# Performance work log

Measured on AMD Instinct MI355X. Metric: run time of the kernel, lower is better.

## Reference

```python
import jax, jax.numpy as jnp
import numpy as np

LN_EPS = 1e-5
SA_EPS = 1e-8
NUM_ITERS = 3

def layer_norm(x, w, b):
    mu = jnp.mean(x, axis=-1, keepdims=True)
    var = jnp.mean((x - mu) ** 2, axis=-1, keepdims=True)
    return (x - mu) / jnp.sqrt(var + LN_EPS) * w + b


def setup_inputs() -> dict:
    key = jax.random.key(0)
    ks = jax.random.split(key, 24)
    B, C, H, W = 128, 256, 32, 32
    D, S, MH, NC = 64, 8, 128, 15
    s = lambda k, shape, scale=0.02: jax.random.normal(k, shape, dtype=jnp.float32) * scale
    inp = {
        "x1": jax.random.normal(ks[0], (B, C, H, W), dtype=jnp.float32),
        "x2": jax.random.normal(ks[1], (B, C, H, W), dtype=jnp.float32),
        # 1x1 convs stored as [out,in]
        "conv1_w": s(ks[2], (D, C)), "conv1_b": jnp.zeros((D,), jnp.float32),
        "conv2_w": s(ks[3], (D, C)), "conv2_b": jnp.zeros((D,), jnp.float32),
        "norm_w": jnp.ones((D,), jnp.float32), "norm_b": jnp.zeros((D,), jnp.float32),
        "ni_w": jnp.ones((D,), jnp.float32), "ni_b": jnp.zeros((D,), jnp.float32),
        "ns_w": jnp.ones((D,), jnp.float32), "ns_b": jnp.zeros((D,), jnp.float32),
        "nm_w": jnp.ones((D,), jnp.float32), "nm_b": jnp.zeros((D,), jnp.float32),
        "slots_mu": s(ks[4], (1, 1, D), 1.0), "slots_log_sigma": s(ks[5], (1, 1, D), 0.1),
        "Wq": s(ks[6], (D, D), 0.1), "Wk": s(ks[7], (D, D), 0.1), "Wv": s(ks[8], (D, D), 0.1),
        "gru_wih": s(ks[9], (3 * D, D), 0.1), "gru_whh": s(ks[10], (3 * D, D), 0.1),
        "gru_bih": jnp.zeros((3 * D,), jnp.float32), "gru_bhh": jnp.zeros((3 * D,), jnp.float32),
        "mlp_w1": s(ks[11], (MH, D), 0.1), "mlp_b1": jnp.zeros((MH,), jnp.float32),
        "mlp_w2": s(ks[12], (D, MH), 0.1), "mlp_b2": jnp.zeros((D,), jnp.float32),
        "head_w": s(ks[13], (NC, D), 0.1), "head_b": jnp.zeros((NC,), jnp.float32),
        "noise": jax.random.normal(ks[14], (B, S, D), dtype=jnp.float32),
    }
    return inp


def _forward(x1, x2, conv1_w, conv1_b, conv2_w, conv2_b, norm_w, norm_b,
             ni_w, ni_b, ns_w, ns_b, nm_w, nm_b, slots_mu, slots_log_sigma,
             Wq, Wk, Wv, gru_wih, gru_whh, gru_bih, gru_bhh,
             mlp_w1, mlp_b1, mlp_w2, mlp_b2, head_w, head_b, noise):
    B = x1.shape[0]
    D = Wq.shape[0]
    # 1x1 convs then flatten to tokens: [B, H*W, D]
    t1 = jnp.einsum('bchw,dc->bhwd', x1, conv1_w).reshape(B, -1, D) + conv1_b
    t2 = jnp.einsum('bchw,dc->bhwd', x2, conv2_w).reshape(B, -1, D) + conv2_b
    inputs = jnp.concatenate([t1, t2], axis=1)          # [B, N, D]
    inputs = layer_norm(inputs, norm_w, norm_b)

    # SlotAttention
    inputs = layer_norm(inputs, ni_w, ni_b)
    k = inputs @ Wk.T                                    # [B, N, D]
    v = inputs @ Wv.T
    slots = slots_mu + jnp.exp(slots_log_sigma) * noise  # [B, S, D]
    scale = D ** -0.5
    for _ in range(NUM_ITERS):
        slots_prev = slots
        sn = layer_norm(slots, ns_w, ns_b)
        q = (sn @ Wq.T) * scale                          # [B, S, D]
        attn_logits = jnp.einsum('bnd,bsd->bns', k, q)   # [B, N, S]
        attn = jax.nn.softmax(attn_logits, axis=-1) + SA_EPS
        attn = attn / jnp.sum(attn, axis=-2, keepdims=True)
        updates = jnp.einsum('bns,bnd->bsd', attn, v)    # [B, S, D]
        # GRUCell (torch gate order: r, z, n)
        gi = updates @ gru_wih.T + gru_bih               # [B, S, 3D]
        gh = slots_prev @ gru_whh.T + gru_bhh
        ir, iz, inn = jnp.split(gi, 3, axis=-1)
        hr, hz, hn = jnp.split(gh, 3, axis=-1)
        r = jax.nn.sigmoid(ir + hr)
        z = jax.nn.sigmoid(iz + hz)
        n = jnp.tanh(inn + r * hn)
        slots = (1.0 - z) * n + z * slots_prev
        # residual MLP
        h = layer_norm(slots, nm_w, nm_b)
        h = jax.nn.relu(h @ mlp_w1.T + mlp_b1) @ mlp_w2.T + mlp_b2
        slots = slots + h

    fused = jnp.mean(slots, axis=1)                      # [B, D]
    return fused @ head_w.T + head_b                     # [B, n_classes]


def reference(x1, x2, conv1_w, conv1_b, conv2_w, conv2_b, norm_w, norm_b,
              ni_w, ni_b, ns_w, ns_b, nm_w, nm_b, slots_mu, slots_log_sigma,
              Wq, Wk, Wv, gru_wih, gru_whh, gru_bih, gru_bhh,
              mlp_w1, mlp_b1, mlp_w2, mlp_b2, head_w, head_b, noise):
    return _forward(x1, x2, conv1_w, conv1_b, conv2_w, conv2_b, norm_w, norm_b,
                    ni_w, ni_b, ns_w, ns_b, nm_w, nm_b, slots_mu, slots_log_sigma,
                    Wq, Wk, Wv, gru_wih, gru_whh, gru_bih, gru_bhh,
                    mlp_w1, mlp_b1, mlp_w2, mlp_b2, head_w, head_b, noise)
```

## Files before the change

kernel.cpp:

```cpp
#include <hip/hip_runtime.h>
#include <stdint.h>


typedef __bf16 bf16;
typedef __bf16 bf16x8 __attribute__((ext_vector_type(8)));
typedef float  f32x4  __attribute__((ext_vector_type(4)));

#define MFMA16(a, b, c) __builtin_amdgcn_mfma_f32_16x16x32_bf16((a), (b), (c), 0, 0, 0)

__global__ __launch_bounds__(256) void k0_convert(
    const float* __restrict__ c1w, const float* __restrict__ c2w,
    const float* __restrict__ wk,  const float* __restrict__ wvv,
    bf16* __restrict__ wconv, bf16* __restrict__ wkv)
{
  const int i = blockIdx.x * 256 + threadIdx.x;
  if (i < 16384) {
    wconv[i]         = (bf16)c1w[i];
    wconv[16384 + i] = (bf16)c2w[i];
  }
  if (i < 4096) {
    wkv[i]        = (bf16)wk[i];
    wkv[4096 + i] = (bf16)wvv[i];
  }
}

__global__ __launch_bounds__(256) void k1_conv_kv(
    const float* __restrict__ x1, const float* __restrict__ x2,
    const float* __restrict__ c1b, const float* __restrict__ c2b,
    const float* __restrict__ nw,  const float* __restrict__ nb,
    const float* __restrict__ niw, const float* __restrict__ nib,
    const bf16* __restrict__ wconv, const bf16* __restrict__ wkv,
    bf16* __restrict__ kbuf, bf16* __restrict__ vT)
{
  __shared__ union {
    struct { float T[64][65]; bf16 tok[64][72]; } p2;
    struct { float Tk[64][65]; float Tv[64][65]; } kv;
  } U;

  const int bx   = blockIdx.x;
  const int tile = bx & 15;
  const int img  = (bx >> 4) & 1;
  const int b    = bx >> 5;
  const int tid  = threadIdx.x;
  const int lane = tid & 63;
  const int wvid = tid >> 6;
  const int l15  = lane & 15;
  const int quad = lane >> 4;

  const float* xp = (img ? x2 : x1) + (size_t)b * (256 * 1024) + tile * 64;
  const bf16* wc  = wconv + img * (64 * 256);
  const int p     = wvid * 16 + l15;
  const float* xcol = xp + p + (size_t)quad * 8 * 1024;

  float xv[64];
  #pragma unroll
  for (int g = 0; g < 8; ++g)
    #pragma unroll
    for (int j = 0; j < 8; ++j)
      xv[g * 8 + j] = xcol[(size_t)(g * 32 + j) * 1024];

  f32x4 acc[4] = {{0.f,0.f,0.f,0.f},{0.f,0.f,0.f,0.f},{0.f,0.f,0.f,0.f},{0.f,0.f,0.f,0.f}};

  #pragma unroll
  for (int g = 0; g < 8; ++g) {
    bf16x8 af;
    #pragma unroll
    for (int j = 0; j < 8; ++j)
      af[j] = (bf16)xv[g * 8 + j];
    #pragma unroll
    for (int nt = 0; nt < 4; ++nt) {
      const bf16x8 bw = *(const bf16x8*)&wc[(nt * 16 + l15) * 256 + g * 32 + quad * 8];
      acc[nt] = MFMA16(af, bw, acc[nt]);
    }
  }

  {
    const float* cb = img ? c2b : c1b;
    #pragma unroll
    for (int nt = 0; nt < 4; ++nt) {
      const int d = nt * 16 + l15;
      const float bias = cb[d];
      #pragma unroll
      for (int r = 0; r < 4; ++r)
        U.p2.T[wvid * 16 + quad * 4 + r][d] = acc[nt][r] + bias;
    }
  }
  __syncthreads();

  {
    const int pix = tid >> 2, part = tid & 3;
    float xv2[16], yv[16];
    float s = 0.f, s2 = 0.f;
    #pragma unroll
    for (int i = 0; i < 16; ++i) {
      xv2[i] = U.p2.T[pix][part * 16 + i];
      s += xv2[i]; s2 += xv2[i] * xv2[i];
    }
    s  += __shfl_xor(s, 1);  s  += __shfl_xor(s, 2);
    s2 += __shfl_xor(s2, 1); s2 += __shfl_xor(s2, 2);
    float mu   = s * 0.015625f;
    float rstd = rsqrtf(s2 * 0.015625f - mu * mu + 1e-5f);
    s = 0.f; s2 = 0.f;
    #pragma unroll
    for (int i = 0; i < 16; ++i) {
      const int d = part * 16 + i;
      const float y = (xv2[i] - mu) * rstd * nw[d] + nb[d];
      yv[i] = y; s += y; s2 += y * y;
    }
    s  += __shfl_xor(s, 1);  s  += __shfl_xor(s, 2);
    s2 += __shfl_xor(s2, 1); s2 += __shfl_xor(s2, 2);
    mu   = s * 0.015625f;
    rstd = rsqrtf(s2 * 0.015625f - mu * mu + 1e-5f);
    #pragma unroll
    for (int i = 0; i < 16; ++i) {
      const int d = part * 16 + i;
      U.p2.tok[pix][d] = (bf16)((yv[i] - mu) * rstd * niw[d] + nib[d]);
    }
  }
  __syncthreads();

  f32x4 ak[4] = {{0.f,0.f,0.f,0.f},{0.f,0.f,0.f,0.f},{0.f,0.f,0.f,0.f},{0.f,0.f,0.f,0.f}};
  f32x4 av[4] = {{0.f,0.f,0.f,0.f},{0.f,0.f,0.f,0.f},{0.f,0.f,0.f,0.f},{0.f,0.f,0.f,0.f}};
  #pragma unroll
  for (int k0 = 0; k0 < 64; k0 += 32) {
    const bf16x8 af = *(const bf16x8*)&U.p2.tok[wvid * 16 + l15][k0 + quad * 8];
    #pragma unroll
    for (int nt = 0; nt < 4; ++nt) {
      const bf16x8 bk = *(const bf16x8*)&wkv[(nt * 16 + l15) * 64 + k0 + quad * 8];
      const bf16x8 bv = *(const bf16x8*)&wkv[4096 + (nt * 16 + l15) * 64 + k0 + quad * 8];
      ak[nt] = MFMA16(af, bk, ak[nt]);
      av[nt] = MFMA16(af, bv, av[nt]);
    }
  }
  __syncthreads();

  #pragma unroll
  for (int nt = 0; nt < 4; ++nt)
    #pragma unroll
    for (int r = 0; r < 4; ++r) {
      U.kv.Tk[wvid * 16 + quad * 4 + r][nt * 16 + l15] = ak[nt][r];
      U.kv.Tv[nt * 16 + l15][wvid * 16 + quad * 4 + r] = av[nt][r];
    }
  __syncthreads();
  {
    const int row = tid >> 2, dd = (tid & 3) * 16;
    const size_t kb = ((size_t)b * 2048 + img * 1024 + tile * 64) * 64;
    bf16 tb[16];
    #pragma unroll
    for (int i = 0; i < 16; ++i) tb[i] = (bf16)U.kv.Tk[row][dd + i];
    *(bf16x8*)&kbuf[kb + (size_t)row * 64 + dd]     = *(bf16x8*)&tb[0];
    *(bf16x8*)&kbuf[kb + (size_t)row * 64 + dd + 8] = *(bf16x8*)&tb[8];
    #pragma unroll
    for (int i = 0; i < 16; ++i) tb[i] = (bf16)U.kv.Tv[row][dd + i];
    const size_t vb = ((size_t)b * 64 + row) * 2048 + img * 1024 + tile * 64 + dd;
    *(bf16x8*)&vT[vb]     = *(bf16x8*)&tb[0];
    *(bf16x8*)&vT[vb + 8] = *(bf16x8*)&tb[8];
  }
}

__global__ __launch_bounds__(512) void kS0(
    const float* __restrict__ smu, const float* __restrict__ slog,
    const float* __restrict__ noise,
    const float* __restrict__ nsw, const float* __restrict__ nsb,
    const float* __restrict__ Wq,
    float* __restrict__ slotbuf, bf16* __restrict__ qbuf)
{
  __shared__ float tmp[8][66];
  const int b = blockIdx.x, tid = threadIdx.x;
  const int s0 = tid >> 6, d0 = tid & 63;
  const int part = tid & 7, sl = (tid >> 3) & 7, wv = tid >> 6;

  const float sval = smu[d0] + expf(slog[d0]) * noise[((size_t)b * 8 + s0) * 64 + d0];
  slotbuf[((size_t)b * 8 + s0) * 64 + d0] = sval;
  float s = sval, s2 = sval * sval;
  #pragma unroll
  for (int m = 1; m < 64; m <<= 1) { s += __shfl_xor(s, m); s2 += __shfl_xor(s2, m); }
  const float mu = s * 0.015625f;
  const float rstd = rsqrtf(s2 * 0.015625f - mu * mu + 1e-5f);
  tmp[s0][d0] = (sval - mu) * rstd * nsw[d0] + nsb[d0];
  __syncthreads();

  float tm[8];
  #pragma unroll
  for (int i = 0; i < 8; ++i) tm[i] = tmp[sl][part * 8 + i];
  for (int orr = 0; orr < 8; ++orr) {
    const int d = orr * 8 + wv;
    const f32x4 w0 = *(const f32x4*)&Wq[d * 64 + part * 8];
    const f32x4 w1v = *(const f32x4*)&Wq[d * 64 + part * 8 + 4];
    float a = tm[0]*w0[0] + tm[1]*w0[1] + tm[2]*w0[2] + tm[3]*w0[3]
            + tm[4]*w1v[0] + tm[5]*w1v[1] + tm[6]*w1v[2] + tm[7]*w1v[3];
    a += __shfl_xor(a, 1); a += __shfl_xor(a, 2); a += __shfl_xor(a, 4);
    if (part == 0) qbuf[((size_t)b * 8 + sl) * 64 + d] = (bf16)(a * 0.125f);
  }
}

__global__ __launch_bounds__(256) void kA(
    const bf16* __restrict__ kbuf, const bf16* __restrict__ vT,
    const bf16* __restrict__ qbuf,
    float* __restrict__ updpart, float* __restrict__ colpart)
{
  __shared__ bf16  qs[16][72];
  __shared__ bf16  attn_b[16][136];
  __shared__ float updp[4][8][64];
  __shared__ float cspart[4][8];

  const int bx  = blockIdx.x;
  const int b   = bx >> 4, ch = bx & 15;
  const int tid = threadIdx.x;
  const int lane = tid & 63, wvid = tid >> 6;
  const int l15 = lane & 15, quad = lane >> 4;
  const size_t tokbase = (size_t)b * 2048 + ch * 128;

  if (tid < 64) {
    const int s = tid >> 3, o = (tid & 7) * 8;
    *(bf16x8*)&qs[s][o] = *(const bf16x8*)&qbuf[((size_t)b * 8 + s) * 64 + o];
  } else if (tid < 128) {
    const int s = 8 + ((tid - 64) >> 3), o = ((tid - 64) & 7) * 8;
    uint32_t* zp = (uint32_t*)&qs[s][o];
    zp[0] = 0u; zp[1] = 0u; zp[2] = 0u; zp[3] = 0u;
  }
  {
    uint32_t* az = (uint32_t*)&attn_b[8][0];
    for (int i = tid; i < 544; i += 256) az[i] = 0u;
  }
  __syncthreads();

  {
    float cs = 0.f;
    #pragma unroll
    for (int mt = 0; mt < 2; ++mt) {
      const int t0 = wvid * 32 + mt * 16;
      const bf16* kr = kbuf + (tokbase + t0 + l15) * 64 + quad * 8;
      f32x4 lg = {0.f, 0.f, 0.f, 0.f};
      lg = MFMA16(*(const bf16x8*)&kr[0],  *(const bf16x8*)&qs[l15][quad * 8],      lg);
      lg = MFMA16(*(const bf16x8*)&kr[32], *(const bf16x8*)&qs[l15][32 + quad * 8], lg);
      #pragma unroll
      for (int r = 0; r < 4; ++r) {
        const float l = lg[r];
        float m = l;
        m = fmaxf(m, __shfl_xor(m, 1));
        m = fmaxf(m, __shfl_xor(m, 2));
        m = fmaxf(m, __shfl_xor(m, 4));
        const float e = expf(l - m);
        float ss = e;
        ss += __shfl_xor(ss, 1);
        ss += __shfl_xor(ss, 2);
        ss += __shfl_xor(ss, 4);
        const float at = e / ss + 1e-8f;
        if (l15 < 8) {
          const bf16 ab = (bf16)at;
          attn_b[l15][t0 + quad * 4 + r] = ab;
          cs += (float)ab;
        }
      }
    }
    cs += __shfl_xor(cs, 16);
    cs += __shfl_xor(cs, 32);
    if (lane < 8) cspart[wvid][lane] = cs;
  }
  __syncthreads();

  {
    const bf16x8 afr = *(const bf16x8*)&attn_b[l15][wvid * 32 + quad * 8];
    const bf16* vrow = vT + (size_t)b * 131072 + (size_t)ch * 128 + wvid * 32 + quad * 8;
    const f32x4 zero4 = {0.f, 0.f, 0.f, 0.f};
    #pragma unroll
    for (int nt = 0; nt < 4; ++nt) {
      const bf16x8 bv = *(const bf16x8*)&vrow[(size_t)(nt * 16 + l15) * 2048];
      f32x4 dd = MFMA16(afr, bv, zero4);
      if (quad < 2) {
        #pragma unroll
        for (int r = 0; r < 4; ++r)
          updp[wvid][quad * 4 + r][nt * 16 + l15] = dd[r];
      }
    }
  }
  __syncthreads();

  {
    const float* up = &updp[0][0][0];
    float* og = updpart + ((size_t)b * 16 + ch) * 512;
    for (int o = tid; o < 512; o += 256)
      og[o] = up[o] + up[o + 512] + up[o + 1024] + up[o + 1536];
    if (tid < 8)
      colpart[((size_t)b * 16 + ch) * 8 + tid] =
        cspart[0][tid] + cspart[1][tid] + cspart[2][tid] + cspart[3][tid];
  }
}

__global__ __launch_bounds__(1024) void kB(
    const float* __restrict__ updpart, const float* __restrict__ colpart,
    float* __restrict__ slotbuf, bf16* __restrict__ qbuf,
    const float* __restrict__ nsw, const float* __restrict__ nsb,
    const float* __restrict__ nmw, const float* __restrict__ nmb,
    const float* __restrict__ Wq,
    const float* __restrict__ wih, const float* __restrict__ whh,
    const float* __restrict__ bih, const float* __restrict__ bhh,
    const float* __restrict__ w1,  const float* __restrict__ b1,
    const float* __restrict__ w2,  const float* __restrict__ b2,
    const float* __restrict__ hwt, const float* __restrict__ hb,
    float* __restrict__ out, const int last)
{
  __shared__ float slots[8][66];
  __shared__ float tmp[8][66];
  __shared__ float gig[8][192], ghg[8][192];
  __shared__ float h1[8][132];
  const int b = blockIdx.x, tid = threadIdx.x;
  const int s0 = (tid >> 6) & 7, d0 = tid & 63;
  const int part = tid & 7, sl = (tid >> 3) & 7;
  const int wv16 = tid >> 6;

  if (tid < 512) {
    const float* up = updpart + (size_t)b * 8192 + s0 * 64 + d0;
    float u = 0.f;
    #pragma unroll
    for (int ch = 0; ch < 16; ++ch) u += up[ch * 512];
    const float* cp = colpart + (size_t)b * 128 + s0;
    float cs = 0.f;
    #pragma unroll
    for (int ch = 0; ch < 16; ++ch) cs += cp[ch * 8];
    tmp[s0][d0] = u / cs;
    slots[s0][d0] = slotbuf[((size_t)b * 8 + s0) * 64 + d0];
  }
  __syncthreads();

  {
    float tv[8], sv[8];
    #pragma unroll
    for (int i = 0; i < 8; ++i) { tv[i] = tmp[sl][part * 8 + i]; sv[i] = slots[sl][part * 8 + i]; }
    for (int jr = 0; jr < 12; ++jr) {
      const int j = jr * 16 + wv16;
      const f32x4 wa0 = *(const f32x4*)&wih[j * 64 + part * 8];
      const f32x4 wa1 = *(const f32x4*)&wih[j * 64 + part * 8 + 4];
      const f32x4 wb0 = *(const f32x4*)&whh[j * 64 + part * 8];
      const f32x4 wb1 = *(const f32x4*)&whh[j * 64 + part * 8 + 4];
      float a = tv[0]*wa0[0] + tv[1]*wa0[1] + tv[2]*wa0[2] + tv[3]*wa0[3]
              + tv[4]*wa1[0] + tv[5]*wa1[1] + tv[6]*wa1[2] + tv[7]*wa1[3];
      float h = sv[0]*wb0[0] + sv[1]*wb0[1] + sv[2]*wb0[2] + sv[3]*wb0[3]
              + sv[4]*wb1[0] + sv[5]*wb1[1] + sv[6]*wb1[2] + sv[7]*wb1[3];
      a += __shfl_xor(a, 1); a += __shfl_xor(a, 2); a += __shfl_xor(a, 4);
      h += __shfl_xor(h, 1); h += __shfl_xor(h, 2); h += __shfl_xor(h, 4);
      if (part == 0) { gig[sl][j] = a + bih[j]; ghg[sl][j] = h + bhh[j]; }
    }
  }
  __syncthreads();

  if (tid < 512) {
    const float r  = 1.f / (1.f + expf(-(gig[s0][d0]       + ghg[s0][d0])));
    const float z  = 1.f / (1.f + expf(-(gig[s0][64 + d0]  + ghg[s0][64 + d0])));
    const float nn = tanhf(gig[s0][128 + d0] + r * ghg[s0][128 + d0]);
    const float snew = (1.f - z) * nn + z * slots[s0][d0];
    slots[s0][d0] = snew;
    float s = snew, s2 = snew * snew;
    #pragma unroll
    for (int m = 1; m < 64; m <<= 1) { s += __shfl_xor(s, m); s2 += __shfl_xor(s2, m); }
    const float mu = s * 0.015625f;
    const float rstd = rsqrtf(s2 * 0.015625f - mu * mu + 1e-5f);
    tmp[s0][d0] = (snew - mu) * rstd * nmw[d0] + nmb[d0];
  }
  __syncthreads();

  {
    float tm[8];
    #pragma unroll
    for (int i = 0; i < 8; ++i) tm[i] = tmp[sl][part * 8 + i];
    for (int jr = 0; jr < 8; ++jr) {
      const int j = jr * 16 + wv16;
      const f32x4 w0 = *(const f32x4*)&w1[j * 64 + part * 8];
      const f32x4 w1v = *(const f32x4*)&w1[j * 64 + part * 8 + 4];
      float a = tm[0]*w0[0] + tm[1]*w0[1] + tm[2]*w0[2] + tm[3]*w0[3]
              + tm[4]*w1v[0] + tm[5]*w1v[1] + tm[6]*w1v[2] + tm[7]*w1v[3];
      a += __shfl_xor(a, 1); a += __shfl_xor(a, 2); a += __shfl_xor(a, 4);
      if (part == 0) h1[sl][j] = fmaxf(a + b1[j], 0.f);
    }
  }
  __syncthreads();

  for (int orr = 0; orr < 4; ++orr) {
    const int d = orr * 16 + wv16;
    float a = 0.f;
    #pragma unroll
    for (int i = 0; i < 4; ++i) {
      const f32x4 wv4 = *(const f32x4*)&w2[d * 128 + part * 16 + i * 4];
      a += h1[sl][part * 16 + i * 4 + 0] * wv4[0] + h1[sl][part * 16 + i * 4 + 1] * wv4[1]
         + h1[sl][part * 16 + i * 4 + 2] * wv4[2] + h1[sl][part * 16 + i * 4 + 3] * wv4[3];
    }
    a += __shfl_xor(a, 1); a += __shfl_xor(a, 2); a += __shfl_xor(a, 4);
    if (part == 0) slots[sl][d] += a + b2[d];
  }
  __syncthreads();

  if (!last) {
    if (tid < 512) {
      const float sfin = slots[s0][d0];
      slotbuf[((size_t)b * 8 + s0) * 64 + d0] = sfin;
      float s = sfin, s2 = sfin * sfin;
      #pragma unroll
      for (int m = 1; m < 64; m <<= 1) { s += __shfl_xor(s, m); s2 += __shfl_xor(s2, m); }
      const float mu = s * 0.015625f;
      const float rstd = rsqrtf(s2 * 0.015625f - mu * mu + 1e-5f);
      tmp[s0][d0] = (sfin - mu) * rstd * nsw[d0] + nsb[d0];
    }
    __syncthreads();
    float tm[8];
    #pragma unroll
    for (int i = 0; i < 8; ++i) tm[i] = tmp[sl][part * 8 + i];
    for (int orr = 0; orr < 4; ++orr) {
      const int d = orr * 16 + wv16;
      const f32x4 w0 = *(const f32x4*)&Wq[d * 64 + part * 8];
      const f32x4 w1v = *(const f32x4*)&Wq[d * 64 + part * 8 + 4];
      float a = tm[0]*w0[0] + tm[1]*w0[1] + tm[2]*w0[2] + tm[3]*w0[3]
              + tm[4]*w1v[0] + tm[5]*w1v[1] + tm[6]*w1v[2] + tm[7]*w1v[3];
      a += __shfl_xor(a, 1); a += __shfl_xor(a, 2); a += __shfl_xor(a, 4);
      if (part == 0) qbuf[((size_t)b * 8 + sl) * 64 + d] = (bf16)(a * 0.125f);
    }
  } else {
    if (tid < 512) slotbuf[((size_t)b * 8 + s0) * 64 + d0] = slots[s0][d0];
    if (tid < 64) {
      float f = 0.f;
      #pragma unroll
      for (int s = 0; s < 8; ++s) f += slots[s][tid];
      tmp[0][tid] = f * 0.125f;
    }
    __syncthreads();
    if (tid < 15) {
      float a = hb[tid];
      for (int d = 0; d < 64; ++d) a += tmp[0][d] * hwt[tid * 64 + d];
      out[b * 15 + tid] = a;
    }
  }
}

extern "C" void kernel_launch(void* const* d_in, const int* in_sizes, int n_in,
                              void* d_out, int out_size, void* d_ws, size_t ws_size,
                              hipStream_t stream) {
  const float* x1   = (const float*)d_in[0];
  const float* x2   = (const float*)d_in[1];
  const float* c1w  = (const float*)d_in[2];
  const float* c1b  = (const float*)d_in[3];
  const float* c2w  = (const float*)d_in[4];
  const float* c2b  = (const float*)d_in[5];
  const float* nw   = (const float*)d_in[6];
  const float* nb   = (const float*)d_in[7];
  const float* niw  = (const float*)d_in[8];
  const float* nib  = (const float*)d_in[9];
  const float* nsw  = (const float*)d_in[10];
  const float* nsb  = (const float*)d_in[11];
  const float* nmw  = (const float*)d_in[12];
  const float* nmb  = (const float*)d_in[13];
  const float* smu  = (const float*)d_in[14];
  const float* slog = (const float*)d_in[15];
  const float* Wq   = (const float*)d_in[16];
  const float* Wk   = (const float*)d_in[17];
  const float* Wv   = (const float*)d_in[18];
  const float* wih  = (const float*)d_in[19];
  const float* whh  = (const float*)d_in[20];
  const float* bih  = (const float*)d_in[21];
  const float* bhh  = (const float*)d_in[22];
  const float* w1   = (const float*)d_in[23];
  const float* b1   = (const float*)d_in[24];
  const float* w2   = (const float*)d_in[25];
  const float* b2   = (const float*)d_in[26];
  const float* hwt  = (const float*)d_in[27];
  const float* hb   = (const float*)d_in[28];
  const float* noise= (const float*)d_in[29];

  char* ws = (char*)d_ws;
  bf16*  kbuf    = (bf16*)(ws);
  bf16*  vT      = (bf16*)(ws + (size_t)33554432);
  bf16*  wconv   = (bf16*)(ws + (size_t)67108864);
  bf16*  wkv     = (bf16*)(ws + (size_t)67174400);
  float* slotbuf = (float*)(ws + (size_t)67190784);
  bf16*  qbuf    = (bf16*)(ws + (size_t)67452928);
  float* updpart = (float*)(ws + (size_t)67584000);
  float* colpart = (float*)(ws + (size_t)71778304);

  k0_convert<<<dim3(64), dim3(256), 0, stream>>>(c1w, c2w, Wk, Wv, wconv, wkv);
  k1_conv_kv<<<dim3(4096), dim3(256), 0, stream>>>(x1, x2, c1b, c2b, nw, nb, niw, nib,
                                                   wconv, wkv, kbuf, vT);
  kS0<<<dim3(128), dim3(512), 0, stream>>>(smu, slog, noise, nsw, nsb, Wq, slotbuf, qbuf);
  for (int it = 0; it < 3; ++it) {
    kA<<<dim3(2048), dim3(256), 0, stream>>>(kbuf, vT, qbuf, updpart, colpart);
    kB<<<dim3(128), dim3(1024), 0, stream>>>(updpart, colpart, slotbuf, qbuf,
                                             nsw, nsb, nmw, nmb, Wq,
                                             wih, whh, bih, bhh, w1, b1, w2, b2,
                                             hwt, hb, (float*)d_out, (it == 2) ? 1 : 0);
  }
}
```

Before: 503.0 us.

## Stage conv input via async global-to-LDS loads and widen pixel tile to 256

The conv/KV kernel now loads channel slabs of the input image straight into LDS with async global_load_lds and uses 1024 blocks, each covering 256 pixels. Previously it used 4096 blocks of 64 pixels with strided per-thread scalar loads. Each block reuses its weight fragments across four 16-pixel subtiles and then runs layernorm plus the K/V projection per 64-pixel chunk, with a permuted pixel mapping on output. This aims to make reads of the 268MB input coalesced and wide. In exchange it adds many more block-level barriers, a larger LDS footprint that may lower occupancy, and fewer blocks in flight.

```diff
diff --git a/kernel.cpp b/kernel.cpp
--- a/kernel.cpp
+++ b/kernel.cpp
@@ -7,6 +7,10 @@
 typedef float  f32x4  __attribute__((ext_vector_type(4)));
 
 #define MFMA16(a, b, c) __builtin_amdgcn_mfma_f32_16x16x32_bf16((a), (b), (c), 0, 0, 0)
+
+#define ASYNC_LDS16(g, l) \
+  __builtin_amdgcn_global_load_lds((const __attribute__((address_space(1))) void*)(g), \
+                                   (__attribute__((address_space(3))) void*)(l), 16, 0, 0)
 
 __global__ __launch_bounds__(256) void k0_convert(
     const float* __restrict__ c1w, const float* __restrict__ c2w,
@@ -33,128 +37,142 @@
     bf16* __restrict__ kbuf, bf16* __restrict__ vT)
 {
   __shared__ union {
+    float xs[32 * 265];
     struct { float T[64][65]; bf16 tok[64][72]; } p2;
     struct { float Tk[64][65]; float Tv[64][65]; } kv;
   } U;
 
-  const int bx   = blockIdx.x;
-  const int tile = bx & 15;
-  const int img  = (bx >> 4) & 1;
-  const int b    = bx >> 5;
-  const int tid  = threadIdx.x;
-  const int lane = tid & 63;
-  const int wvid = tid >> 6;
-  const int l15  = lane & 15;
-  const int quad = lane >> 4;
-
-  const float* xp = (img ? x2 : x1) + (size_t)b * (256 * 1024) + tile * 64;
+  const int bx    = blockIdx.x;
+  const int ptile = bx & 3;
+  const int img   = (bx >> 2) & 1;
+  const int b     = bx >> 3;
+  const int tid   = threadIdx.x;
+  const int lane  = tid & 63;
+  const int wvid  = tid >> 6;
+  const int l15   = lane & 15;
+  const int quad  = lane >> 4;
+
+  const float* xp = (img ? x2 : x1) + (size_t)b * (256 * 1024) + ptile * 256;
   const bf16* wc  = wconv + img * (64 * 256);
-  const int p     = wvid * 16 + l15;
-  const float* xcol = xp + p + (size_t)quad * 8 * 1024;
-
-  float xv[64];
+
+  f32x4 acc[4][4];
   #pragma unroll
-  for (int g = 0; g < 8; ++g)
-    #pragma unroll
-    for (int j = 0; j < 8; ++j)
-      xv[g * 8 + j] = xcol[(size_t)(g * 32 + j) * 1024];
-
-  f32x4 acc[4] = {{0.f,0.f,0.f,0.f},{0.f,0.f,0.f,0.f},{0.f,0.f,0.f,0.f},{0.f,0.f,0.f,0.f}};
-
-  #pragma unroll
-  for (int g = 0; g < 8; ++g) {
-    bf16x8 af;
-    #pragma unroll
-    for (int j = 0; j < 8; ++j)
-      af[j] = (bf16)xv[g * 8 + j];
-    #pragma unroll
-    for (int nt = 0; nt < 4; ++nt) {
-      const bf16x8 bw = *(const bf16x8*)&wc[(nt * 16 + l15) * 256 + g * 32 + quad * 8];
-      acc[nt] = MFMA16(af, bw, acc[nt]);
-    }
-  }
-
-  {
-    const float* cb = img ? c2b : c1b;
+  for (int m = 0; m < 4; ++m)
+    #pragma unroll
+    for (int nt = 0; nt < 4; ++nt)
+      acc[m][nt] = (f32x4){0.f, 0.f, 0.f, 0.f};
+
+  for (int h = 0; h < 8; ++h) {
+    #pragma unroll
+    for (int i = 0; i < 8; ++i) {
+      const int cl = wvid * 8 + i;
+      ASYNC_LDS16(xp + (size_t)(h * 32 + cl) * 1024 + lane * 4, &U.xs[cl * 265]);
+    }
+    __syncthreads();
+
+    bf16x8 bw[4];
+    #pragma unroll
+    for (int nt = 0; nt < 4; ++nt)
+      bw[nt] = *(const bf16x8*)&wc[(nt * 16 + l15) * 256 + h * 32 + quad * 8];
+    #pragma unroll
+    for (int m = 0; m < 4; ++m) {
+      bf16x8 af;
+      #pragma unroll
+      for (int j = 0; j < 8; ++j)
+        af[j] = (bf16)U.xs[(quad * 8 + j) * 265 + wvid * 64 + m * 16 + l15];
+      #pragma unroll
+      for (int nt = 0; nt < 4; ++nt)
+        acc[m][nt] = MFMA16(af, bw[nt], acc[m][nt]);
+    }
+    __syncthreads();
+  }
+
+  const float* cb = img ? c2b : c1b;
+  const size_t tokbase = (size_t)b * 2048 + img * 1024 + ptile * 256;
+
+  for (int m = 0; m < 4; ++m) {
     #pragma unroll
     for (int nt = 0; nt < 4; ++nt) {
       const int d = nt * 16 + l15;
       const float bias = cb[d];
       #pragma unroll
       for (int r = 0; r < 4; ++r)
-        U.p2.T[wvid * 16 + quad * 4 + r][d] = acc[nt][r] + bias;
-    }
-  }
-  __syncthreads();
-
-  {
-    const int pix = tid >> 2, part = tid & 3;
-    float xv2[16], yv[16];
-    float s = 0.f, s2 = 0.f;
-    #pragma unroll
-    for (int i = 0; i < 16; ++i) {
-      xv2[i] = U.p2.T[pix][part * 16 + i];
-      s += xv2[i]; s2 += xv2[i] * xv2[i];
-    }
-    s  += __shfl_xor(s, 1);  s  += __shfl_xor(s, 2);
-    s2 += __shfl_xor(s2, 1); s2 += __shfl_xor(s2, 2);
-    float mu   = s * 0.015625f;
-    float rstd = rsqrtf(s2 * 0.015625f - mu * mu + 1e-5f);
-    s = 0.f; s2 = 0.f;
-    #pragma unroll
-    for (int i = 0; i < 16; ++i) {
-      const int d = part * 16 + i;
-      const float y = (xv2[i] - mu) * rstd * nw[d] + nb[d];
-      yv[i] = y; s += y; s2 += y * y;
-    }
-    s  += __shfl_xor(s, 1);  s  += __shfl_xor(s, 2);
-    s2 += __shfl_xor(s2, 1); s2 += __shfl_xor(s2, 2);
-    mu   = s * 0.015625f;
-    rstd = rsqrtf(s2 * 0.015625f - mu * mu + 1e-5f);
-    #pragma unroll
-    for (int i = 0; i < 16; ++i) {
-      const int d = part * 16 + i;
-      U.p2.tok[pix][d] = (bf16)((yv[i] - mu) * rstd * niw[d] + nib[d]);
-    }
-  }
-  __syncthreads();
-
-  f32x4 ak[4] = {{0.f,0.f,0.f,0.f},{0.f,0.f,0.f,0.f},{0.f,0.f,0.f,0.f},{0.f,0.f,0.f,0.f}};
-  f32x4 av[4] = {{0.f,0.f,0.f,0.f},{0.f,0.f,0.f,0.f},{0.f,0.f,0.f,0.f},{0.f,0.f,0.f,0.f}};
-  #pragma unroll
-  for (int k0 = 0; k0 < 64; k0 += 32) {
-    const bf16x8 af = *(const bf16x8*)&U.p2.tok[wvid * 16 + l15][k0 + quad * 8];
-    #pragma unroll
-    for (int nt = 0; nt < 4; ++nt) {
-      const bf16x8 bk = *(const bf16x8*)&wkv[(nt * 16 + l15) * 64 + k0 + quad * 8];
-      const bf16x8 bv = *(const bf16x8*)&wkv[4096 + (nt * 16 + l15) * 64 + k0 + quad * 8];
-      ak[nt] = MFMA16(af, bk, ak[nt]);
-      av[nt] = MFMA16(af, bv, av[nt]);
-    }
-  }
-  __syncthreads();
-
-  #pragma unroll
-  for (int nt = 0; nt < 4; ++nt)
-    #pragma unroll
-    for (int r = 0; r < 4; ++r) {
-      U.kv.Tk[wvid * 16 + quad * 4 + r][nt * 16 + l15] = ak[nt][r];
-      U.kv.Tv[nt * 16 + l15][wvid * 16 + quad * 4 + r] = av[nt][r];
-    }
-  __syncthreads();
-  {
-    const int row = tid >> 2, dd = (tid & 3) * 16;
-    const size_t kb = ((size_t)b * 2048 + img * 1024 + tile * 64) * 64;
-    bf16 tb[16];
-    #pragma unroll
-    for (int i = 0; i < 16; ++i) tb[i] = (bf16)U.kv.Tk[row][dd + i];
-    *(bf16x8*)&kbuf[kb + (size_t)row * 64 + dd]     = *(bf16x8*)&tb[0];
-    *(bf16x8*)&kbuf[kb + (size_t)row * 64 + dd + 8] = *(bf16x8*)&tb[8];
-    #pragma unroll
-    for (int i = 0; i < 16; ++i) tb[i] = (bf16)U.kv.Tv[row][dd + i];
-    const size_t vb = ((size_t)b * 64 + row) * 2048 + img * 1024 + tile * 64 + dd;
-    *(bf16x8*)&vT[vb]     = *(bf16x8*)&tb[0];
-    *(bf16x8*)&vT[vb + 8] = *(bf16x8*)&tb[8];
+        U.p2.T[wvid * 16 + quad * 4 + r][d] = acc[m][nt][r] + bias;
+    }
+    __syncthreads();
+
+    {
+      const int pix = tid >> 2, part = tid & 3;
+      float xv[16], yv[16];
+      float s = 0.f, s2 = 0.f;
+      #pragma unroll
+      for (int i = 0; i < 16; ++i) {
+        xv[i] = U.p2.T[pix][part * 16 + i];
+        s += xv[i]; s2 += xv[i] * xv[i];
+      }
+      s  += __shfl_xor(s, 1);  s  += __shfl_xor(s, 2);
+      s2 += __shfl_xor(s2, 1); s2 += __shfl_xor(s2, 2);
+      float mu   = s * 0.015625f;
+      float rstd = rsqrtf(s2 * 0.015625f - mu * mu + 1e-5f);
+      s = 0.f; s2 = 0.f;
+      #pragma unroll
+      for (int i = 0; i < 16; ++i) {
+        const int d = part * 16 + i;
+        const float y = (xv[i] - mu) * rstd * nw[d] + nb[d];
+        yv[i] = y; s += y; s2 += y * y;
+      }
+      s  += __shfl_xor(s, 1);  s  += __shfl_xor(s, 2);
+      s2 += __shfl_xor(s2, 1); s2 += __shfl_xor(s2, 2);
+      mu   = s * 0.015625f;
+      rstd = rsqrtf(s2 * 0.015625f - mu * mu + 1e-5f);
+      #pragma unroll
+      for (int i = 0; i < 16; ++i) {
+        const int d = part * 16 + i;
+        U.p2.tok[pix][d] = (bf16)((yv[i] - mu) * rstd * niw[d] + nib[d]);
+      }
+    }
+    __syncthreads();
+
+    f32x4 ak[4] = {{0.f,0.f,0.f,0.f},{0.f,0.f,0.f,0.f},{0.f,0.f,0.f,0.f},{0.f,0.f,0.f,0.f}};
+    f32x4 av[4] = {{0.f,0.f,0.f,0.f},{0.f,0.f,0.f,0.f},{0.f,0.f,0.f,0.f},{0.f,0.f,0.f,0.f}};
+    #pragma unroll
+    for (int k0 = 0; k0 < 64; k0 += 32) {
+      const bf16x8 af = *(const bf16x8*)&U.p2.tok[wvid * 16 + l15][k0 + quad * 8];
+      #pragma unroll
+      for (int nt = 0; nt < 4; ++nt) {
+        const bf16x8 bk = *(const bf16x8*)&wkv[(nt * 16 + l15) * 64 + k0 + quad * 8];
+        const bf16x8 bv = *(const bf16x8*)&wkv[4096 + (nt * 16 + l15) * 64 + k0 + quad * 8];
+        ak[nt] = MFMA16(af, bk, ak[nt]);
+        av[nt] = MFMA16(af, bv, av[nt]);
+      }
+    }
+    __syncthreads();
+
+    #pragma unroll
+    for (int nt = 0; nt < 4; ++nt)
+      #pragma unroll
+      for (int r = 0; r < 4; ++r) {
+        U.kv.Tk[wvid * 16 + quad * 4 + r][nt * 16 + l15] = ak[nt][r];
+        U.kv.Tv[nt * 16 + l15][wvid * 16 + quad * 4 + r] = av[nt][r];
+      }
+    __syncthreads();
+
+    {
+      const int row = tid >> 2, dd = (tid & 3) * 16;
+      bf16 tb[16];
+      const int pxk = (row >> 4) * 64 + m * 16 + (row & 15);
+      #pragma unroll
+      for (int i = 0; i < 16; ++i) tb[i] = (bf16)U.kv.Tk[row][dd + i];
+      *(bf16x8*)&kbuf[(tokbase + pxk) * 64 + dd]     = *(bf16x8*)&tb[0];
+      *(bf16x8*)&kbuf[(tokbase + pxk) * 64 + dd + 8] = *(bf16x8*)&tb[8];
+      #pragma unroll
+      for (int i = 0; i < 16; ++i) tb[i] = (bf16)U.kv.Tv[row][dd + i];
+      const int pxv = (dd >> 4) * 64 + m * 16;
+      const size_t vb = ((size_t)b * 64 + row) * 2048 + img * 1024 + ptile * 256 + pxv;
+      *(bf16x8*)&vT[vb]     = *(bf16x8*)&tb[0];
+      *(bf16x8*)&vT[vb + 8] = *(bf16x8*)&tb[8];
+    }
+    __syncthreads();
   }
 }
 
@@ -476,7 +494,7 @@
   float* colpart = (float*)(ws + (size_t)71778304);
 
   k0_convert<<<dim3(64), dim3(256), 0, stream>>>(c1w, c2w, Wk, Wv, wconv, wkv);
-  k1_conv_kv<<<dim3(4096), dim3(256), 0, stream>>>(x1, x2, c1b, c2b, nw, nb, niw, nib,
+  k1_conv_kv<<<dim3(1024), dim3(256), 0, stream>>>(x1, x2, c1b, c2b, nw, nb, niw, nib,
                                                    wconv, wkv, kbuf, vT);
   kS0<<<dim3(128), dim3(512), 0, stream>>>(smu, slog, noise, nsw, nsb, Wq, slotbuf, qbuf);
   for (int it = 0; it < 3; ++it) {
```

Measured after the change: 517.1 us. 2.8% more time.
